# Optimization experiments

Measured on AMD Instinct MI355X. Metric: run time of the kernel, lower is better.

Reference implementation:

```python
import jax, jax.numpy as jnp
import numpy as np

SMOOTHING = 0.2
CONFIDENCE = 1.0 - SMOOTHING


def setup_inputs() -> dict:
    key = jax.random.key(0)
    k1, k2 = jax.random.split(key)
    B, C = 4096, 50257
    pred = jax.random.normal(k1, (B, C), dtype=jnp.float32)
    target = jax.random.randint(k2, (B,), 0, C, dtype=jnp.int64)
    return {"pred": pred, "target": target}


def reference(pred, target):
    # pred: [B, C] logits, target: [B] int class ids
    B, C = pred.shape
    logp = jax.nn.log_softmax(pred, axis=-1)  # [B, C]
    t = target
    rows = jnp.arange(B)
    # Gather log-probs at target and its two neighbors (clipped at edges).
    lp_t = logp[rows, t]
    lp_l = logp[rows, jnp.clip(t - 1, 0, C - 1)]
    lp_r = logp[rows, jnp.clip(t + 1, 0, C - 1)]
    # Neighbor smoothing weights, matching the original per-sample branching:
    #   t == 0    -> all smoothing mass on t+1
    #   t == C-1  -> all smoothing mass on t-1
    #   otherwise -> smoothing/2 on each neighbor
    w_l = jnp.where(t == 0, 0.0, jnp.where(t == C - 1, SMOOTHING, SMOOTHING / 2))
    w_r = jnp.where(t == 0, SMOOTHING, jnp.where(t == C - 1, 0.0, SMOOTHING / 2))
    loss_i = -(CONFIDENCE * lp_t + w_l * lp_l + w_r * lp_r)  # [B]
    return jnp.mean(loss_i)
```

## Files before the change

### kernel.cpp

```cpp
#include <hip/hip_runtime.h>
#include <math.h>

#define SMOOTHING_F  0.2f
#define CONFIDENCE_F 0.8f

typedef float f32x4 __attribute__((ext_vector_type(4)));


__global__ __launch_bounds__(256)
void row_loss_kernel(const float* __restrict__ pred,
                     const int* __restrict__ target,
                     float* __restrict__ row_loss,
                     int C) {
    const int row = blockIdx.x;
    const int tid = threadIdx.x;
    const float* p = pred + (size_t)row * (size_t)C;

    float s0 = 0.0f, s1 = 0.0f, s2 = 0.0f, s3 = 0.0f;

    const int misalign = (int)(((size_t)row * (size_t)C) & 3);
    const int lead = (4 - misalign) & 3;

    const f32x4* vp = (const f32x4*)(p + lead);
    const int nv = (C - lead) >> 2;

    int v = tid;
    for (; v + 256 < nv; v += 512) {
        f32x4 x = __builtin_nontemporal_load(&vp[v]);
        f32x4 y = __builtin_nontemporal_load(&vp[v + 256]);
        s0 += __expf(x.x); s1 += __expf(x.y);
        s2 += __expf(x.z); s3 += __expf(x.w);
        s0 += __expf(y.x); s1 += __expf(y.y);
        s2 += __expf(y.z); s3 += __expf(y.w);
    }
    if (v < nv) {
        f32x4 x = __builtin_nontemporal_load(&vp[v]);
        s0 += __expf(x.x); s1 += __expf(x.y);
        s2 += __expf(x.z); s3 += __expf(x.w);
    }
    if (tid < lead) s0 += __expf(p[tid]);
    const int tail_start = lead + (nv << 2);
    const int tail = C - tail_start;
    if (tid < tail) s0 += __expf(p[tail_start + tid]);

    float s = (s0 + s1) + (s2 + s3);

    #pragma unroll
    for (int i = 1; i < 64; i <<= 1) s += __shfl_xor(s, i, 64);

    __shared__ float smem_s[4];
    const int wave = tid >> 6;
    if ((tid & 63) == 0) smem_s[wave] = s;
    __syncthreads();

    if (tid == 0) {
        const float S = (smem_s[0] + smem_s[1]) + (smem_s[2] + smem_s[3]);
        const float logZ = logf(S);

        const int t  = target[row];
        const int tl = max(t - 1, 0);
        const int tr = min(t + 1, C - 1);
        const float pt = p[t];
        const float pl = p[tl];
        const float pr = p[tr];

        float wl, wr;
        if (t == 0)            { wl = 0.0f;               wr = SMOOTHING_F; }
        else if (t == C - 1)   { wl = SMOOTHING_F;        wr = 0.0f; }
        else                   { wl = 0.5f * SMOOTHING_F; wr = 0.5f * SMOOTHING_F; }

        row_loss[row] = logZ - (CONFIDENCE_F * pt + wl * pl + wr * pr);
    }
}

__global__ __launch_bounds__(256)
void reduce_mean_kernel(const float* __restrict__ row_loss,
                        float* __restrict__ out, int B) {
    float acc = 0.0f;
    for (int i = threadIdx.x; i < B; i += 256) acc += row_loss[i];
    #pragma unroll
    for (int i = 1; i < 64; i <<= 1) acc += __shfl_xor(acc, i, 64);
    __shared__ float sacc[4];
    const int wave = threadIdx.x >> 6;
    if ((threadIdx.x & 63) == 0) sacc[wave] = acc;
    __syncthreads();
    if (threadIdx.x == 0) {
        out[0] = (sacc[0] + sacc[1] + sacc[2] + sacc[3]) / (float)B;
    }
}

extern "C" void kernel_launch(void* const* d_in, const int* in_sizes, int n_in,
                              void* d_out, int out_size, void* d_ws, size_t ws_size,
                              hipStream_t stream) {
    const float* pred  = (const float*)d_in[0];
    const int* target  = (const int*)d_in[1];
    float* out         = (float*)d_out;
    float* row_loss    = (float*)d_ws;

    const int B = in_sizes[1];
    const int C = in_sizes[0] / in_sizes[1];

    row_loss_kernel<<<B, 256, 0, stream>>>(pred, target, row_loss, C);
    reduce_mean_kernel<<<1, 256, 0, stream>>>(row_loss, out, B);
}
```

Measured before the change: 136.5 us.

## Fuse final mean reduction into row kernel via last-block ticket; unroll loads by four

Merges the separate mean-reduction kernel into the per-row kernel. Each block publishes its row loss and takes a ticket from an atomic counter, and the last block to finish sums all row losses. The main loop also now issues four vector loads per iteration instead of two, to keep more memory requests in flight. The fusion removes one kernel launch but adds a memset launch, a device-wide fence and an atomic per block.

```diff
diff --git a/kernel.cpp b/kernel.cpp
--- a/kernel.cpp
+++ b/kernel.cpp
@@ -8,10 +8,12 @@
 
 
 __global__ __launch_bounds__(256)
-void row_loss_kernel(const float* __restrict__ pred,
-                     const int* __restrict__ target,
-                     float* __restrict__ row_loss,
-                     int C) {
+void fused_loss_kernel(const float* __restrict__ pred,
+                       const int* __restrict__ target,
+                       float* __restrict__ row_loss,
+                       unsigned int* __restrict__ ticket,
+                       float* __restrict__ out,
+                       int C, int B) {
     const int row = blockIdx.x;
     const int tid = threadIdx.x;
     const float* p = pred + (size_t)row * (size_t)C;
@@ -25,18 +27,19 @@
     const int nv = (C - lead) >> 2;
 
     int v = tid;
-    for (; v + 256 < nv; v += 512) {
-        f32x4 x = __builtin_nontemporal_load(&vp[v]);
-        f32x4 y = __builtin_nontemporal_load(&vp[v + 256]);
-        s0 += __expf(x.x); s1 += __expf(x.y);
-        s2 += __expf(x.z); s3 += __expf(x.w);
-        s0 += __expf(y.x); s1 += __expf(y.y);
-        s2 += __expf(y.z); s3 += __expf(y.w);
+    for (; v + 768 < nv; v += 1024) {
+        f32x4 a = __builtin_nontemporal_load(&vp[v]);
+        f32x4 b = __builtin_nontemporal_load(&vp[v + 256]);
+        f32x4 c = __builtin_nontemporal_load(&vp[v + 512]);
+        f32x4 d = __builtin_nontemporal_load(&vp[v + 768]);
+        s0 += __expf(a.x); s1 += __expf(a.y); s2 += __expf(a.z); s3 += __expf(a.w);
+        s0 += __expf(b.x); s1 += __expf(b.y); s2 += __expf(b.z); s3 += __expf(b.w);
+        s0 += __expf(c.x); s1 += __expf(c.y); s2 += __expf(c.z); s3 += __expf(c.w);
+        s0 += __expf(d.x); s1 += __expf(d.y); s2 += __expf(d.z); s3 += __expf(d.w);
     }
-    if (v < nv) {
-        f32x4 x = __builtin_nontemporal_load(&vp[v]);
-        s0 += __expf(x.x); s1 += __expf(x.y);
-        s2 += __expf(x.z); s3 += __expf(x.w);
+    for (; v < nv; v += 256) {
+        f32x4 a = __builtin_nontemporal_load(&vp[v]);
+        s0 += __expf(a.x); s1 += __expf(a.y); s2 += __expf(a.z); s3 += __expf(a.w);
     }
     if (tid < lead) s0 += __expf(p[tid]);
     const int tail_start = lead + (nv << 2);
@@ -49,6 +52,7 @@
     for (int i = 1; i < 64; i <<= 1) s += __shfl_xor(s, i, 64);
 
     __shared__ float smem_s[4];
+    __shared__ int last_flag;
     const int wave = tid >> 6;
     if ((tid & 63) == 0) smem_s[wave] = s;
     __syncthreads();
@@ -69,23 +73,30 @@
         else if (t == C - 1)   { wl = SMOOTHING_F;        wr = 0.0f; }
         else                   { wl = 0.5f * SMOOTHING_F; wr = 0.5f * SMOOTHING_F; }
 
-        row_loss[row] = logZ - (CONFIDENCE_F * pt + wl * pl + wr * pr);
+        const float loss = logZ - (CONFIDENCE_F * pt + wl * pl + wr * pr);
+        __hip_atomic_store(&row_loss[row], loss, __ATOMIC_RELAXED,
+                           __HIP_MEMORY_SCOPE_AGENT);
+
+        __threadfence();
+        unsigned int old = atomicAdd(ticket, 1u);
+        last_flag = (old == (unsigned int)(B - 1)) ? 1 : 0;
     }
-}
+    __syncthreads();
 
-__global__ __launch_bounds__(256)
-void reduce_mean_kernel(const float* __restrict__ row_loss,
-                        float* __restrict__ out, int B) {
-    float acc = 0.0f;
-    for (int i = threadIdx.x; i < B; i += 256) acc += row_loss[i];
-    #pragma unroll
-    for (int i = 1; i < 64; i <<= 1) acc += __shfl_xor(acc, i, 64);
-    __shared__ float sacc[4];
-    const int wave = threadIdx.x >> 6;
-    if ((threadIdx.x & 63) == 0) sacc[wave] = acc;
-    __syncthreads();
-    if (threadIdx.x == 0) {
-        out[0] = (sacc[0] + sacc[1] + sacc[2] + sacc[3]) / (float)B;
+    if (last_flag) {
+        __threadfence();
+        float acc = 0.0f;
+        for (int i = tid; i < B; i += 256)
+            acc += __hip_atomic_load(&row_loss[i], __ATOMIC_RELAXED,
+                                     __HIP_MEMORY_SCOPE_AGENT);
+        #pragma unroll
+        for (int i = 1; i < 64; i <<= 1) acc += __shfl_xor(acc, i, 64);
+        __shared__ float sacc[4];
+        if ((tid & 63) == 0) sacc[tid >> 6] = acc;
+        __syncthreads();
+        if (tid == 0) {
+            out[0] = (sacc[0] + sacc[1] + sacc[2] + sacc[3]) / (float)B;
+        }
     }
 }
 
@@ -95,11 +106,13 @@
     const float* pred  = (const float*)d_in[0];
     const int* target  = (const int*)d_in[1];
     float* out         = (float*)d_out;
-    float* row_loss    = (float*)d_ws;
 
     const int B = in_sizes[1];
     const int C = in_sizes[0] / in_sizes[1];
 
-    row_loss_kernel<<<B, 256, 0, stream>>>(pred, target, row_loss, C);
-    reduce_mean_kernel<<<1, 256, 0, stream>>>(row_loss, out, B);
+    float* row_loss      = (float*)d_ws;
+    unsigned int* ticket = (unsigned int*)((char*)d_ws + (size_t)B * sizeof(float));
+
+    hipMemsetAsync(ticket, 0, sizeof(unsigned int), stream);
+    fused_loss_kernel<<<B, 256, 0, stream>>>(pred, target, row_loss, ticket, out, C, B);
 }
```

Measured after the change: 344.5 us. 2.52x slower.
